# Performance work log

Hardware: AMD Instinct MI355X
Metric: run time of the kernel (lower is better)

The kernel has to match this reference:

```python
import jax, jax.numpy as jnp
import numpy as np

N_KERNELS = 21
N_LAYERS = 2
N_HEADS = 8
ATT_DIM = 32
FF_HID = 100
EMB = 300


def kernel_mus(n):
    mus = [1.0]
    bin_size = 2.0 / (n - 1)
    mus.append(1.0 - bin_size / 2.0)
    for _ in range(1, n - 1):
        mus.append(mus[-1] - bin_size)
    return np.array(mus, dtype=np.float32)


def kernel_sigmas(n):
    return np.array([0.001] + [0.1] * (n - 1), dtype=np.float32)


def setup_inputs() -> dict:
    key = jax.random.key(0)
    ks = jax.random.split(key, 12)
    B, LQ, LD = 32, 64, 512
    u = lambda k, s, a: jax.random.uniform(k, s, jnp.float32, -a, a)
    return dict(
        q_embed=jax.random.normal(ks[0], (B, LQ, EMB), jnp.float32),
        d_embed=jax.random.normal(ks[1], (B, LD, EMB), jnp.float32),
        mask_q=(jax.random.uniform(ks[2], (B, LQ)) > 0.1).astype(jnp.float32),
        mask_d=(jax.random.uniform(ks[3], (B, LD)) > 0.1).astype(jnp.float32),
        mixer=jnp.full((1, 1, 1), 0.5, jnp.float32),
        nn_scaler=jnp.full((1,), 0.01, jnp.float32),
        ff_w1=u(ks[4], (N_LAYERS, EMB, FF_HID), 0.05),
        ff_b1=jnp.zeros((N_LAYERS, FF_HID), jnp.float32),
        ff_w2=u(ks[5], (N_LAYERS, FF_HID, EMB), 0.05),
        ff_b2=jnp.zeros((N_LAYERS, EMB), jnp.float32),
        ln1_g=jnp.ones((N_LAYERS, EMB), jnp.float32),
        ln1_b=jnp.zeros((N_LAYERS, EMB), jnp.float32),
        att_w=u(ks[6], (N_LAYERS, EMB, 3 * ATT_DIM), 0.05),
        att_b=jnp.zeros((N_LAYERS, 3 * ATT_DIM), jnp.float32),
        out_w=u(ks[7], (N_LAYERS, ATT_DIM, EMB), 0.05),
        out_b=jnp.zeros((N_LAYERS, EMB), jnp.float32),
        ln2_g=jnp.ones((N_LAYERS, EMB), jnp.float32),
        ln2_b=jnp.zeros((N_LAYERS, EMB), jnp.float32),
        dense_w=u(ks[8], (1, N_KERNELS), 0.014),
    )


def _layer_norm(x, g, b, eps=1e-6):
    m = jnp.mean(x, -1, keepdims=True)
    s = jnp.std(x, -1, keepdims=True, ddof=1)  # torch std is unbiased
    return g * (x - m) / (s + eps) + b


def _encoder(x, mask, p):
    # AllenNLP StackedSelfAttentionEncoder: [FF -> res+LN -> MHSA -> res+LN] x2
    B, T, E = x.shape
    scale = jnp.sqrt(jnp.float32(E // N_HEADS))
    hd = ATT_DIM // N_HEADS
    for l in range(N_LAYERS):
        h = jax.nn.relu(x @ p['ff_w1'][l] + p['ff_b1'][l]) @ p['ff_w2'][l] + p['ff_b2'][l]
        h = _layer_norm(h + x, p['ln1_g'][l], p['ln1_b'][l])
        c = h @ p['att_w'][l] + p['att_b'][l]              # [B,T,3*ATT_DIM]
        q = c[..., :ATT_DIM].reshape(B, T, N_HEADS, hd)
        k = c[..., ATT_DIM:2 * ATT_DIM].reshape(B, T, N_HEADS, hd)
        v = c[..., 2 * ATT_DIM:].reshape(B, T, N_HEADS, hd)
        sims = jnp.einsum('bqhd,bkhd->bhqk', q / scale, k)
        m = mask[:, None, None, :]
        att = jax.nn.softmax(sims * m, axis=-1) * m         # AllenNLP masked_softmax
        att = att / (jnp.sum(att, -1, keepdims=True) + 1e-13)
        o = jnp.einsum('bhqk,bkhd->bqhd', att, v).reshape(B, T, ATT_DIM)
        o = o @ p['out_w'][l] + p['out_b'][l]
        x = _layer_norm(o + h, p['ln2_g'][l], p['ln2_b'][l])
    return x


def reference(q_embed, d_embed, mask_q, mask_d, mixer, nn_scaler,
              ff_w1, ff_b1, ff_w2, ff_b2, ln1_g, ln1_b,
              att_w, att_b, out_w, out_b, ln2_g, ln2_b, dense_w):
    p = dict(ff_w1=ff_w1, ff_b1=ff_b1, ff_w2=ff_w2, ff_b2=ff_b2,
             ln1_g=ln1_g, ln1_b=ln1_b, att_w=att_w, att_b=att_b,
             out_w=out_w, out_b=out_b, ln2_g=ln2_g, ln2_b=ln2_b)
    mu = jnp.asarray(kernel_mus(N_KERNELS))        # [K]
    sigma = jnp.asarray(kernel_sigmas(N_KERNELS))  # [K]
    mq = mask_q[..., None]
    md = mask_d[..., None]
    q = q_embed * mq
    d = d_embed * md
    qc = _encoder(q, mask_q, p)
    dc = _encoder(d, mask_d, p)
    q = (mixer * q + (1.0 - mixer) * qc) * mq
    d = (mixer * d + (1.0 - mixer) * dc) * md
    qd_mask = mask_q[:, :, None] * mask_d[:, None, :]  # [B,Q,D]
    qn = q / (jnp.linalg.norm(q, axis=-1, keepdims=True) + 1e-13)
    dn = d / (jnp.linalg.norm(d, axis=-1, keepdims=True) + 1e-13)
    cos = jnp.einsum('bqe,bde->bqd', qn, dn) * qd_mask
    # Gaussian RBF soft histogram: [B,Q,D,K]
    kr = jnp.exp(-(cos[..., None] - mu) ** 2 / (2.0 * sigma ** 2)) * qd_mask[..., None]
    pkq = jnp.sum(kr, axis=2)                                 # [B,Q,K]
    log_pkq = jnp.log2(jnp.clip(pkq, 1e-10)) * nn_scaler
    per_kernel = jnp.sum(log_pkq * mq, axis=1)                # [B,K]
    return jnp.squeeze(per_kernel @ dense_w.T, axis=1)        # [B]
```

## Files before the change

kernel.cpp:

```cpp
#include <hip/hip_runtime.h>
#include <hip/hip_bf16.h>

#define BATCH 32
#define LQ 64
#define LD 512
#define EMB 300
#define FFH 100
#define ATTD 32
#define NH 8
#define NK 21
#define MQ (BATCH * LQ)
#define MD (BATCH * LD)
#define MALL (MQ + MD)

typedef __attribute__((ext_vector_type(8))) short bf16x8;
typedef __attribute__((ext_vector_type(4))) float f32x4;

__device__ __forceinline__ float wave_sum(float v) {
    #pragma unroll
    for (int off = 32; off > 0; off >>= 1) v += __shfl_xor(v, off);
    return v;
}

__device__ __forceinline__ float bf2f(__hip_bfloat16 h) { return __bfloat162float(h); }

__device__ __forceinline__ float4 bf4_to_f4(const __hip_bfloat16* p) {
    uint2 u = *(const uint2*)p;
    float4 f;
    f.x = __uint_as_float((u.x & 0xffffu) << 16);
    f.y = __uint_as_float(u.x & 0xffff0000u);
    f.z = __uint_as_float((u.y & 0xffffu) << 16);
    f.w = __uint_as_float(u.y & 0xffff0000u);
    return f;
}

__device__ __forceinline__ unsigned short f2bfu(float x) {
    __hip_bfloat16 h = __float2bfloat16(x);
    return *(unsigned short*)&h;
}

__global__ void prep_all(const float* __restrict__ qe, const float* __restrict__ de,
                         const float* __restrict__ mq, const float* __restrict__ md,
                         const float* __restrict__ w1, const float* __restrict__ w2,
                         const float* __restrict__ aw, const float* __restrict__ ow,
                         __hip_bfloat16* __restrict__ xbf, float* __restrict__ mall,
                         __hip_bfloat16* __restrict__ w1t, __hip_bfloat16* __restrict__ w2t,
                         __hip_bfloat16* __restrict__ awt, __hip_bfloat16* __restrict__ owt) {
    int i = blockIdx.x * blockDim.x + threadIdx.x;
    const int NQ4 = MALL * (EMB / 4);
    if (i < NQ4) {
        int tok = i / (EMB / 4), c4 = (i % (EMB / 4)) * 4;
        float m;
        float4 v;
        if (tok < MQ) {
            m = mq[tok];
            v = *(const float4*)(qe + (size_t)tok * EMB + c4);
        } else {
            m = md[tok - MQ];
            v = *(const float4*)(de + (size_t)(tok - MQ) * EMB + c4);
        }
        uint2 u;
        u.x = (unsigned)f2bfu(v.x * m) | ((unsigned)f2bfu(v.y * m) << 16);
        u.y = (unsigned)f2bfu(v.z * m) | ((unsigned)f2bfu(v.w * m) << 16);
        *(uint2*)(xbf + (size_t)tok * EMB + c4) = u;
        if (c4 == 0) mall[tok] = m;
        return;
    }
    int j = i - NQ4;
    if (j < 2 * EMB * FFH) {
        int l = j / (EMB * FFH), r = j % (EMB * FFH);
        int k = r / FFH, n = r % FFH;
        w1t[(size_t)l * FFH * EMB + (size_t)n * EMB + k] = __float2bfloat16(w1[j]);
        return;
    }
    j -= 2 * EMB * FFH;
    if (j < 2 * 320 * 128) {
        int l = j / (320 * 128), r = j % (320 * 128);
        int n = r / 128, k = r % 128;
        float v = (n < EMB && k < FFH) ? w2[(size_t)l * FFH * EMB + (size_t)k * EMB + n] : 0.f;
        w2t[j] = __float2bfloat16(v);
        return;
    }
    j -= 2 * 320 * 128;
    if (j < 2 * EMB * 96) {
        int l = j / (EMB * 96), r = j % (EMB * 96);
        int k = r / 96, n = r % 96;
        awt[(size_t)l * 96 * EMB + (size_t)n * EMB + k] = __float2bfloat16(aw[j]);
        return;
    }
    j -= 2 * EMB * 96;
    if (j < 2 * 320 * 32) {
        int l = j / (320 * 32), r = j % (320 * 32);
        int n = r / 32, k = r % 32;
        float v = (n < EMB) ? ow[(size_t)l * ATTD * EMB + (size_t)k * EMB + n] : 0.f;
        owt[j] = __float2bfloat16(v);
    }
}

__device__ __forceinline__ void stage_row8(const __hip_bfloat16* __restrict__ src, bool rowvalid,
                                           int K, int gk, __hip_bfloat16* dst) {
    if (rowvalid && gk + 8 <= K) {
        const uint2* p = (const uint2*)(src + gk);
        uint2 a = p[0], b = p[1];
        *(uint2*)dst = a;
        *(uint2*)(dst + 4) = b;
    } else {
        #pragma unroll
        for (int j = 0; j < 8; j++)
            dst[j] = (rowvalid && gk + j < K) ? src[gk + j] : __float2bfloat16(0.f);
    }
}

template <bool RELU>
__global__ __launch_bounds__(256) void gemm_mfma(const __hip_bfloat16* __restrict__ A,
                                                 const __hip_bfloat16* __restrict__ Bt,
                                                 const float* __restrict__ bias,
                                                 __hip_bfloat16* __restrict__ Cb,
                                                 int M, int Nr, int Ns, int K) {
    __shared__ __align__(16) __hip_bfloat16 As[64][40];
    __shared__ __align__(16) __hip_bfloat16 Bs[64][40];
    const int tid = threadIdx.x;
    const int m0 = blockIdx.y * 64, n0 = blockIdx.x * 64;
    const int lane = tid & 63;
    const int wv = tid >> 6;
    const int wm = wv >> 1, wn = wv & 1;
    const int l15 = lane & 15, lg = lane >> 4;
    const int srow = tid >> 2, sk8 = (tid & 3) * 8;
    f32x4 acc[2][2] = {};
    const int NS = (K + 31) >> 5;
    const __hip_bfloat16* arow = A + (size_t)(m0 + srow) * K;
    const bool bvalid = (n0 + srow) < Nr;
    const __hip_bfloat16* brow = Bt + (size_t)(n0 + srow) * K;

    for (int s = 0; s < NS; s++) {
        const int gk = (s << 5) + sk8;
        if (s) __syncthreads();
        stage_row8(arow, true, K, gk, &As[srow][sk8]);
        stage_row8(brow, bvalid, K, gk, &Bs[srow][sk8]);
        __syncthreads();
        bf16x8 af0 = *(const bf16x8*)&As[wm * 32 + l15][lg * 8];
        bf16x8 af1 = *(const bf16x8*)&As[wm * 32 + 16 + l15][lg * 8];
        bf16x8 bf0 = *(const bf16x8*)&Bs[wn * 32 + l15][lg * 8];
        bf16x8 bf1 = *(const bf16x8*)&Bs[wn * 32 + 16 + l15][lg * 8];
        acc[0][0] = __builtin_amdgcn_mfma_f32_16x16x32_bf16(af0, bf0, acc[0][0], 0, 0, 0);
        acc[0][1] = __builtin_amdgcn_mfma_f32_16x16x32_bf16(af0, bf1, acc[0][1], 0, 0, 0);
        acc[1][0] = __builtin_amdgcn_mfma_f32_16x16x32_bf16(af1, bf0, acc[1][0], 0, 0, 0);
        acc[1][1] = __builtin_amdgcn_mfma_f32_16x16x32_bf16(af1, bf1, acc[1][1], 0, 0, 0);
    }

    #pragma unroll
    for (int fc = 0; fc < 2; fc++) {
        int col = n0 + wn * 32 + fc * 16 + l15;
        if (col >= Ns) continue;
        float bs = (col < Nr) ? bias[col] : 0.f;
        #pragma unroll
        for (int fr = 0; fr < 2; fr++) {
            int rbase = m0 + wm * 32 + fr * 16 + lg * 4;
            #pragma unroll
            for (int r = 0; r < 4; r++) {
                float v = acc[fr][fc][r] + bs;
                if (RELU) v = fmaxf(v, 0.f);
                Cb[(size_t)(rbase + r) * Ns + col] = __float2bfloat16(v);
            }
        }
    }
}

template <int NSTEP, int KSTR, int ASTR, bool MIX>
__global__ __launch_bounds__(256) void gemm_ln_direct(const __hip_bfloat16* __restrict__ A,
                                                      const __hip_bfloat16* __restrict__ Bt,
                                                      const float* __restrict__ bias,
                                                      const __hip_bfloat16* __restrict__ Res,
                                                      const float* __restrict__ g,
                                                      const float* __restrict__ beta,
                                                      __hip_bfloat16* __restrict__ Y,
                                                      const __hip_bfloat16* __restrict__ Xorig,
                                                      const float* __restrict__ mall,
                                                      const float* __restrict__ mixer) {
    const int tid = threadIdx.x;
    const int wv = tid >> 6;
    const int lane = tid & 63;
    const int l15 = lane & 15, lg = lane >> 4;
    const int m0 = blockIdx.x * 64 + wv * 16;

    f32x4 acc[19];
    #pragma unroll
    for (int fc = 0; fc < 19; fc++) acc[fc] = (f32x4){0.f, 0.f, 0.f, 0.f};

    #pragma unroll
    for (int ks = 0; ks < NSTEP; ks++) {
        const int kb = ks * 32 + lg * 8;
        bf16x8 af = *(const bf16x8*)(A + (size_t)(m0 + l15) * ASTR + kb);
        #pragma unroll
        for (int fc = 0; fc < 19; fc++) {
            bf16x8 bf = *(const bf16x8*)(Bt + (size_t)(fc * 16 + l15) * KSTR + kb);
            acc[fc] = __builtin_amdgcn_mfma_f32_16x16x32_bf16(af, bf, acc[fc], 0, 0, 0);
        }
    }

    float rs[4] = {0.f, 0.f, 0.f, 0.f};
    #pragma unroll
    for (int fc = 0; fc < 19; fc++) {
        int col = fc * 16 + l15;
        bool valid = col < EMB;
        float bs = valid ? bias[col] : 0.f;
        #pragma unroll
        for (int r = 0; r < 4; r++) {
            float v = 0.f;
            if (valid) v = acc[fc][r] + bs + bf2f(Res[(size_t)(m0 + lg * 4 + r) * EMB + col]);
            acc[fc][r] = v;
            rs[r] += v;
        }
    }
    #pragma unroll
    for (int r = 0; r < 4; r++)
        #pragma unroll
        for (int off = 1; off < 16; off <<= 1)
            rs[r] += __shfl_xor(rs[r], off);
    float mean[4], invv[4];
    #pragma unroll
    for (int r = 0; r < 4; r++) mean[r] = rs[r] * (1.f / EMB);

    float rq[4] = {0.f, 0.f, 0.f, 0.f};
    #pragma unroll
    for (int fc = 0; fc < 19; fc++) {
        int col = fc * 16 + l15;
        if (col < EMB) {
            #pragma unroll
            for (int r = 0; r < 4; r++) {
                float d = acc[fc][r] - mean[r];
                rq[r] += d * d;
            }
        }
    }
    #pragma unroll
    for (int r = 0; r < 4; r++) {
        #pragma unroll
        for (int off = 1; off < 16; off <<= 1)
            rq[r] += __shfl_xor(rq[r], off);
        float stdv = sqrtf(rq[r] * (1.f / (EMB - 1)));
        invv[r] = 1.f / (stdv + 1e-6f);
    }

    if (!MIX) {
        #pragma unroll
        for (int fc = 0; fc < 19; fc++) {
            int col = fc * 16 + l15;
            if (col >= EMB) continue;
            float gv = g[col], bv = beta[col];
            #pragma unroll
            for (int r = 0; r < 4; r++) {
                float y = gv * (acc[fc][r] - mean[r]) * invv[r] + bv;
                Y[(size_t)(m0 + lg * 4 + r) * EMB + col] = __float2bfloat16(y);
            }
        }
    } else {
        float mx = mixer[0];
        float mval[4];
        #pragma unroll
        for (int r = 0; r < 4; r++) mval[r] = mall[m0 + lg * 4 + r];
        float sq[4] = {0.f, 0.f, 0.f, 0.f};
        #pragma unroll
        for (int fc = 0; fc < 19; fc++) {
            int col = fc * 16 + l15;
            bool valid = col < EMB;
            float gv = valid ? g[col] : 0.f;
            float bv = valid ? beta[col] : 0.f;
            #pragma unroll
            for (int r = 0; r < 4; r++) {
                float v = 0.f;
                if (valid) {
                    float ln = gv * (acc[fc][r] - mean[r]) * invv[r] + bv;
                    float xo = bf2f(Xorig[(size_t)(m0 + lg * 4 + r) * EMB + col]);
                    v = (mx * xo + (1.f - mx) * ln) * mval[r];
                }
                acc[fc][r] = v;
                sq[r] += v * v;
            }
        }
        #pragma unroll
        for (int r = 0; r < 4; r++) {
            #pragma unroll
            for (int off = 1; off < 16; off <<= 1)
                sq[r] += __shfl_xor(sq[r], off);
            sq[r] = 1.f / (sqrtf(sq[r]) + 1e-13f);
        }
        #pragma unroll
        for (int fc = 0; fc < 19; fc++) {
            int col = fc * 16 + l15;
            if (col >= EMB) continue;
            #pragma unroll
            for (int r = 0; r < 4; r++) {
                Y[(size_t)(m0 + lg * 4 + r) * EMB + col] = __float2bfloat16(acc[fc][r] * sq[r]);
            }
        }
    }
}

__global__ __launch_bounds__(256) void cos_mfma(const __hip_bfloat16* __restrict__ Qn,
                                                const __hip_bfloat16* __restrict__ Dn,
                                                float* __restrict__ Cos) {
    __shared__ __align__(16) __hip_bfloat16 As[64][40];
    __shared__ __align__(16) __hip_bfloat16 Bs[64][40];
    const int b = blockIdx.y;
    const int n0 = blockIdx.x * 64;
    const int tid = threadIdx.x;
    const int lane = tid & 63;
    const int wv = tid >> 6;
    const int wm = wv >> 1, wn = wv & 1;
    const int l15 = lane & 15, lg = lane >> 4;
    const int srow = tid >> 2, sk8 = (tid & 3) * 8;
    f32x4 acc[2][2] = {};
    const int NS = (EMB + 31) >> 5;
    const __hip_bfloat16* arow = Qn + ((size_t)b * LQ + srow) * EMB;
    const __hip_bfloat16* brow = Dn + ((size_t)b * LD + n0 + srow) * EMB;

    for (int s = 0; s < NS; s++) {
        const int gk = (s << 5) + sk8;
        if (s) __syncthreads();
        stage_row8(arow, true, EMB, gk, &As[srow][sk8]);
        stage_row8(brow, true, EMB, gk, &Bs[srow][sk8]);
        __syncthreads();
        bf16x8 af0 = *(const bf16x8*)&As[wm * 32 + l15][lg * 8];
        bf16x8 af1 = *(const bf16x8*)&As[wm * 32 + 16 + l15][lg * 8];
        bf16x8 bf0 = *(const bf16x8*)&Bs[wn * 32 + l15][lg * 8];
        bf16x8 bf1 = *(const bf16x8*)&Bs[wn * 32 + 16 + l15][lg * 8];
        acc[0][0] = __builtin_amdgcn_mfma_f32_16x16x32_bf16(af0, bf0, acc[0][0], 0, 0, 0);
        acc[0][1] = __builtin_amdgcn_mfma_f32_16x16x32_bf16(af0, bf1, acc[0][1], 0, 0, 0);
        acc[1][0] = __builtin_amdgcn_mfma_f32_16x16x32_bf16(af1, bf0, acc[1][0], 0, 0, 0);
        acc[1][1] = __builtin_amdgcn_mfma_f32_16x16x32_bf16(af1, bf1, acc[1][1], 0, 0, 0);
    }

    float* cb = Cos + (size_t)b * LQ * LD;
    #pragma unroll
    for (int fc = 0; fc < 2; fc++) {
        int col = n0 + wn * 32 + fc * 16 + l15;
        #pragma unroll
        for (int fr = 0; fr < 2; fr++) {
            int rbase = wm * 32 + fr * 16 + lg * 4;
            #pragma unroll
            for (int r = 0; r < 4; r++) {
                cb[(size_t)(rbase + r) * LD + col] = acc[fr][fc][r];
            }
        }
    }
}

template <int T, int RPB, int KS>
__device__ __forceinline__ void attn_body(const __hip_bfloat16* __restrict__ cseg,
                                          const float* __restrict__ mask,
                                          __hip_bfloat16* __restrict__ oseg,
                                          int bh, int rb, char* smem) {
    constexpr int BLK = 512;
    float4* Ks = (float4*)smem;
    float4* Vs = Ks + T;
    float* part = (float*)(Vs + T);
    float* nmask_s = part + RPB * 5 * (KS - 1);
    const int b = bh / NH, h = bh % NH;
    const int tid = threadIdx.x;
    const __hip_bfloat16* base = cseg + (size_t)b * T * 96;

    if (tid == 0) *nmask_s = 0.f;
    __syncthreads();
    float lnm = 0.f;
    for (int j = tid; j < T; j += BLK) {
        float m = mask[b * T + j];
        float4 kv = bf4_to_f4(base + (size_t)j * 96 + ATTD + h * 4);
        float4 vv = bf4_to_f4(base + (size_t)j * 96 + 2 * ATTD + h * 4);
        kv.x *= m; kv.y *= m; kv.z *= m; kv.w *= m;
        vv.x *= m; vv.y *= m; vv.z *= m; vv.w *= m;
        Ks[j] = kv;
        Vs[j] = vv;
        lnm += 1.f - m;
    }
    lnm = wave_sum(lnm);
    if ((tid & 63) == 0 && lnm != 0.f) atomicAdd(nmask_s, lnm);
    __syncthreads();

    const int r = rb * RPB + (tid % RPB);
    const int ks = tid / RPB;
    const float inv_scale = 0.16439898730535729f;
    float4 qv = bf4_to_f4(base + (size_t)r * 96 + h * 4);
    qv.x *= inv_scale; qv.y *= inv_scale; qv.z *= inv_scale; qv.w *= inv_scale;

    float Sall = 0.f, ox = 0.f, oy = 0.f, oz = 0.f, ow = 0.f;
    constexpr int KC = T / KS;
    const int k0 = ks * KC;
    #pragma unroll 4
    for (int k = k0; k < k0 + KC; k++) {
        float4 kv = Ks[k];
        float4 vv = Vs[k];
        float s = fmaf(qv.x, kv.x, fmaf(qv.y, kv.y, fmaf(qv.z, kv.z, qv.w * kv.w)));
        float e = __expf(s);
        Sall += e;
        ox = fmaf(e, vv.x, ox);
        oy = fmaf(e, vv.y, oy);
        oz = fmaf(e, vv.z, oz);
        ow = fmaf(e, vv.w, ow);
    }
    if (ks > 0) {
        float* p = &part[((ks - 1) * RPB + (tid % RPB)) * 5];
        p[0] = Sall; p[1] = ox; p[2] = oy; p[3] = oz; p[4] = ow;
    }
    __syncthreads();
    if (ks == 0) {
        #pragma unroll
        for (int s2 = 0; s2 < KS - 1; s2++) {
            const float* p = &part[(s2 * RPB + r - rb * RPB) * 5];
            Sall += p[0]; ox += p[1]; oy += p[2]; oz += p[3]; ow += p[4];
        }
        float Sm = Sall - *nmask_s;
        float inv = 1.f / (Sm + 1e-13f * Sall);
        __hip_bfloat16* op = oseg + (size_t)(b * T + r) * ATTD + h * 4;
        op[0] = __float2bfloat16(ox * inv);
        op[1] = __float2bfloat16(oy * inv);
        op[2] = __float2bfloat16(oz * inv);
        op[3] = __float2bfloat16(ow * inv);
    }
}

__global__ __launch_bounds__(512) void attn_both(const __hip_bfloat16* __restrict__ cbf,
                                                 const float* __restrict__ mask_q,
                                                 const float* __restrict__ mask_d,
                                                 __hip_bfloat16* __restrict__ o32) {
    __shared__ __align__(16) char smem[24576];
    int blk = blockIdx.x;
    if (blk < BATCH * NH) {
        attn_body<LQ, 64, 8>(cbf, mask_q, o32, blk, 0, smem);
    } else {
        int bid = blk - BATCH * NH;
        attn_body<LD, 128, 4>(cbf + (size_t)MQ * 96, mask_d, o32 + (size_t)MQ * ATTD,
                              bid >> 2, bid & 3, smem);
    }
}

__global__ __launch_bounds__(256) void pool_kernel(const float* __restrict__ Cos,
                                                   const float* __restrict__ mask_q,
                                                   const float* __restrict__ mask_d,
                                                   const float* __restrict__ nn_scaler,
                                                   float* __restrict__ lp) {
    int wid = (blockIdx.x * 256 + threadIdx.x) >> 6;
    int lane = threadIdx.x & 63;
    int b = wid >> 6, qi = wid & 63;
    const float* crow = Cos + ((size_t)b * LQ + qi) * LD;
    const float* md = mask_d + b * LD;
    float acc[NK];
    #pragma unroll
    for (int k = 0; k < NK; k++) acc[k] = 0.f;
    #pragma unroll
    for (int rr = 0; rr < LD / 64; rr++) {
        int dj = rr * 64 + lane;
        float m = md[dj];
        if (m != 0.f) {
            float cv = crow[dj];
            float d0 = cv - 1.0f;
            acc[0] += __expf(d0 * d0 * -500000.0f);
            #pragma unroll
            for (int g = 0; g < 4; g++) {
                float mu_a = 0.95f - 0.5f * g;
                float dc = cv - mu_a;
                float t = __expf(dc * dc * -50.0f);
                float r = __expf(fmaf(-10.0f, dc, -0.5f));
                #pragma unroll
                for (int j = 0; j < 5; j++) {
                    acc[1 + 5 * g + j] += t;
                    t *= r;
                    r *= 0.36787944117144233f;
                }
            }
        }
    }
    float mq = mask_q[b * LQ + qi];
    float ns = nn_scaler[0];
    #pragma unroll
    for (int k = 0; k < NK; k++) {
        float s = wave_sum(acc[k]);
        if (lane == 0) lp[((size_t)b * LQ + qi) * NK + k] = log2f(fmaxf(s, 1e-10f)) * ns * mq;
    }
}

__global__ void final_kernel(const float* __restrict__ lp, const float* __restrict__ dense_w,
                             float* __restrict__ out) {
    int b = blockIdx.x;
    int t = threadIdx.x;
    float s = 0.f;
    if (t < NK) {
        for (int qi = 0; qi < LQ; qi++) s += lp[((size_t)b * LQ + qi) * NK + t];
        s *= dense_w[t];
    }
    s = wave_sum(s);
    if (t == 0) out[b] = s;
}

extern "C" void kernel_launch(void* const* d_in, const int* in_sizes, int n_in,
                              void* d_out, int out_size, void* d_ws, size_t ws_size,
                              hipStream_t stream) {
    (void)in_sizes; (void)n_in; (void)out_size; (void)ws_size;
    const float* q_embed  = (const float*)d_in[0];
    const float* d_embed  = (const float*)d_in[1];
    const float* mask_q   = (const float*)d_in[2];
    const float* mask_d   = (const float*)d_in[3];
    const float* mixer    = (const float*)d_in[4];
    const float* nn_scaler= (const float*)d_in[5];
    const float* ff_w1    = (const float*)d_in[6];
    const float* ff_b1    = (const float*)d_in[7];
    const float* ff_w2    = (const float*)d_in[8];
    const float* ff_b2    = (const float*)d_in[9];
    const float* ln1_g    = (const float*)d_in[10];
    const float* ln1_b    = (const float*)d_in[11];
    const float* att_w    = (const float*)d_in[12];
    const float* att_b    = (const float*)d_in[13];
    const float* out_w    = (const float*)d_in[14];
    const float* out_b    = (const float*)d_in[15];
    const float* ln2_g    = (const float*)d_in[16];
    const float* ln2_b    = (const float*)d_in[17];
    const float* dense_w  = (const float*)d_in[18];
    float* out = (float*)d_out;

    float* ws   = (float*)d_ws;
    float* cosb = ws;
    float* lp   = cosb + 1048576;
    float* mall = lp + 43008;
    __hip_bfloat16* xbf   = (__hip_bfloat16*)(mall + MALL);
    __hip_bfloat16* xcbf  = xbf  + (size_t)MALL * EMB;
    __hip_bfloat16* qdn   = xcbf + (size_t)MALL * EMB;
    __hip_bfloat16* hbf   = qdn  + (size_t)MALL * EMB;
    __hip_bfloat16* t1bf  = hbf  + (size_t)MALL * EMB;
    __hip_bfloat16* cbf   = t1bf + (size_t)MALL * 128;
    __hip_bfloat16* o32bf = cbf  + (size_t)MALL * 96;
    __hip_bfloat16* w1t   = o32bf + (size_t)MALL * ATTD;
    __hip_bfloat16* w2t   = w1t + 2 * FFH * EMB;
    __hip_bfloat16* awt   = w2t + 2 * 320 * 128;
    __hip_bfloat16* owt   = awt + 2 * 96 * EMB;

    const int PREP_N = MALL * (EMB / 4) + 2 * EMB * FFH + 2 * 320 * 128 + 2 * EMB * 96 + 2 * 320 * 32;
    prep_all<<<(PREP_N + 255) / 256, 256, 0, stream>>>(
        q_embed, d_embed, mask_q, mask_d, ff_w1, ff_w2, att_w, out_w,
        xbf, mall, w1t, w2t, awt, owt);

    const __hip_bfloat16* xcur = xbf;
    for (int l = 0; l < 2; l++) {
        gemm_mfma<true><<<dim3(2, MALL / 64), 256, 0, stream>>>(
            xcur, w1t + (size_t)l * FFH * EMB, ff_b1 + l * FFH, t1bf, MALL, FFH, 128, EMB);
        gemm_ln_direct<4, 128, 128, false><<<MALL / 64, 256, 0, stream>>>(
            t1bf, w2t + (size_t)l * 320 * 128, ff_b2 + l * EMB, xcur,
            ln1_g + l * EMB, ln1_b + l * EMB, hbf, nullptr, nullptr, nullptr);
        gemm_mfma<false><<<dim3(2, MALL / 64), 256, 0, stream>>>(
            hbf, awt + (size_t)l * 96 * EMB, att_b + l * 96, cbf, MALL, 96, 96, EMB);
        attn_both<<<BATCH * NH + BATCH * NH * (LD / 128), 512, 0, stream>>>(
            cbf, mask_q, mask_d, o32bf);
        if (l == 0) {
            gemm_ln_direct<1, 32, 32, false><<<MALL / 64, 256, 0, stream>>>(
                o32bf, owt, out_b, hbf, ln2_g, ln2_b, xcbf, nullptr, nullptr, nullptr);
            xcur = xcbf;
        } else {
            gemm_ln_direct<1, 32, 32, true><<<MALL / 64, 256, 0, stream>>>(
                o32bf, owt + (size_t)320 * 32, out_b + EMB, hbf,
                ln2_g + EMB, ln2_b + EMB, qdn, xbf, mall, mixer);
        }
    }

    cos_mfma<<<dim3(LD / 64, BATCH), 256, 0, stream>>>(qdn, qdn + (size_t)MQ * EMB, cosb);

    pool_kernel<<<(BATCH * LQ) / 4, 256, 0, stream>>>(cosb, mask_q, mask_d, nn_scaler, lp);

    final_kernel<<<BATCH, 64, 0, stream>>>(lp, dense_w, out);
}
```

Measured before the change: 233.3 us.

## Store cosine matrix in bf16 and fuse final reduction into pool via atomic counter

The cosine similarity matrix is now written and read as bf16 instead of fp32, halving that intermediate's memory traffic. The final dense reduction kernel is removed. The last wave per batch, found with an atomic counter that prep_all resets, does the dense dot product inside the pool kernel, saving one launch. This risks precision loss in the RBF histogram, where sigma=0.001 for the exact-match kernel makes bf16 rounding of cos near 1 significant.

```diff
diff --git a/kernel.cpp b/kernel.cpp
--- a/kernel.cpp
+++ b/kernel.cpp
@@ -45,7 +45,8 @@
                          const float* __restrict__ aw, const float* __restrict__ ow,
                          __hip_bfloat16* __restrict__ xbf, float* __restrict__ mall,
                          __hip_bfloat16* __restrict__ w1t, __hip_bfloat16* __restrict__ w2t,
-                         __hip_bfloat16* __restrict__ awt, __hip_bfloat16* __restrict__ owt) {
+                         __hip_bfloat16* __restrict__ awt, __hip_bfloat16* __restrict__ owt,
+                         int* __restrict__ cnt) {
     int i = blockIdx.x * blockDim.x + threadIdx.x;
     const int NQ4 = MALL * (EMB / 4);
     if (i < NQ4) {
@@ -94,7 +95,10 @@
         int n = r / 32, k = r % 32;
         float v = (n < EMB) ? ow[(size_t)l * ATTD * EMB + (size_t)k * EMB + n] : 0.f;
         owt[j] = __float2bfloat16(v);
-    }
+        return;
+    }
+    j -= 2 * 320 * 32;
+    if (j < BATCH) cnt[j] = 0;
 }
 
 __device__ __forceinline__ void stage_row8(const __hip_bfloat16* __restrict__ src, bool rowvalid,
@@ -299,7 +303,7 @@
 
 __global__ __launch_bounds__(256) void cos_mfma(const __hip_bfloat16* __restrict__ Qn,
                                                 const __hip_bfloat16* __restrict__ Dn,
-                                                float* __restrict__ Cos) {
+                                                __hip_bfloat16* __restrict__ Cos) {
     __shared__ __align__(16) __hip_bfloat16 As[64][40];
     __shared__ __align__(16) __hip_bfloat16 Bs[64][40];
     const int b = blockIdx.y;
@@ -331,7 +335,7 @@
         acc[1][1] = __builtin_amdgcn_mfma_f32_16x16x32_bf16(af1, bf1, acc[1][1], 0, 0, 0);
     }
 
-    float* cb = Cos + (size_t)b * LQ * LD;
+    __hip_bfloat16* cb = Cos + (size_t)b * LQ * LD;
     #pragma unroll
     for (int fc = 0; fc < 2; fc++) {
         int col = n0 + wn * 32 + fc * 16 + l15;
@@ -340,7 +344,7 @@
             int rbase = wm * 32 + fr * 16 + lg * 4;
             #pragma unroll
             for (int r = 0; r < 4; r++) {
-                cb[(size_t)(rbase + r) * LD + col] = acc[fr][fc][r];
+                cb[(size_t)(rbase + r) * LD + col] = __float2bfloat16(acc[fr][fc][r]);
             }
         }
     }
@@ -434,15 +438,18 @@
     }
 }
 
-__global__ __launch_bounds__(256) void pool_kernel(const float* __restrict__ Cos,
-                                                   const float* __restrict__ mask_q,
-                                                   const float* __restrict__ mask_d,
-                                                   const float* __restrict__ nn_scaler,
-                                                   float* __restrict__ lp) {
+__global__ __launch_bounds__(256) void pool_final(const __hip_bfloat16* __restrict__ Cos,
+                                                  const float* __restrict__ mask_q,
+                                                  const float* __restrict__ mask_d,
+                                                  const float* __restrict__ nn_scaler,
+                                                  const float* __restrict__ dense_w,
+                                                  float* __restrict__ lp,
+                                                  int* __restrict__ cnt,
+                                                  float* __restrict__ out) {
     int wid = (blockIdx.x * 256 + threadIdx.x) >> 6;
     int lane = threadIdx.x & 63;
     int b = wid >> 6, qi = wid & 63;
-    const float* crow = Cos + ((size_t)b * LQ + qi) * LD;
+    const __hip_bfloat16* crow = Cos + ((size_t)b * LQ + qi) * LD;
     const float* md = mask_d + b * LD;
     float acc[NK];
     #pragma unroll
@@ -452,7 +459,7 @@
         int dj = rr * 64 + lane;
         float m = md[dj];
         if (m != 0.f) {
-            float cv = crow[dj];
+            float cv = bf2f(crow[dj]);
             float d0 = cv - 1.0f;
             acc[0] += __expf(d0 * d0 * -500000.0f);
             #pragma unroll
@@ -477,19 +484,20 @@
         float s = wave_sum(acc[k]);
         if (lane == 0) lp[((size_t)b * LQ + qi) * NK + k] = log2f(fmaxf(s, 1e-10f)) * ns * mq;
     }
-}
-
-__global__ void final_kernel(const float* __restrict__ lp, const float* __restrict__ dense_w,
-                             float* __restrict__ out) {
-    int b = blockIdx.x;
-    int t = threadIdx.x;
-    float s = 0.f;
-    if (t < NK) {
-        for (int qi = 0; qi < LQ; qi++) s += lp[((size_t)b * LQ + qi) * NK + t];
-        s *= dense_w[t];
-    }
-    s = wave_sum(s);
-    if (t == 0) out[b] = s;
+
+    __threadfence();
+    int old = 0;
+    if (lane == 0) old = atomicAdd(&cnt[b], 1);
+    old = __shfl(old, 0);
+    if (old == LQ - 1) {
+        __threadfence();
+        const float* lpb = lp + (size_t)b * LQ * NK;
+        float t = 0.f;
+        #pragma unroll
+        for (int k = 0; k < NK; k++) t += lpb[(size_t)lane * NK + k] * dense_w[k];
+        t = wave_sum(t);
+        if (lane == 0) out[b] = t;
+    }
 }
 
 extern "C" void kernel_launch(void* const* d_in, const int* in_sizes, int n_in,
@@ -518,10 +526,11 @@
     float* out = (float*)d_out;
 
     float* ws   = (float*)d_ws;
-    float* cosb = ws;
-    float* lp   = cosb + 1048576;
+    float* lp   = ws;
     float* mall = lp + 43008;
-    __hip_bfloat16* xbf   = (__hip_bfloat16*)(mall + MALL);
+    int*   cnt  = (int*)(mall + MALL);
+    __hip_bfloat16* cosbf = (__hip_bfloat16*)(cnt + BATCH);
+    __hip_bfloat16* xbf   = cosbf + (size_t)BATCH * LQ * LD;
     __hip_bfloat16* xcbf  = xbf  + (size_t)MALL * EMB;
     __hip_bfloat16* qdn   = xcbf + (size_t)MALL * EMB;
     __hip_bfloat16* hbf   = qdn  + (size_t)MALL * EMB;
@@ -533,10 +542,11 @@
     __hip_bfloat16* awt   = w2t + 2 * 320 * 128;
     __hip_bfloat16* owt   = awt + 2 * 96 * EMB;
 
-    const int PREP_N = MALL * (EMB / 4) + 2 * EMB * FFH + 2 * 320 * 128 + 2 * EMB * 96 + 2 * 320 * 32;
+    const int PREP_N = MALL * (EMB / 4) + 2 * EMB * FFH + 2 * 320 * 128 + 2 * EMB * 96
+                     + 2 * 320 * 32 + BATCH;
     prep_all<<<(PREP_N + 255) / 256, 256, 0, stream>>>(
         q_embed, d_embed, mask_q, mask_d, ff_w1, ff_w2, att_w, out_w,
-        xbf, mall, w1t, w2t, awt, owt);
+        xbf, mall, w1t, w2t, awt, owt, cnt);
 
     const __hip_bfloat16* xcur = xbf;
     for (int l = 0; l < 2; l++) {
@@ -560,9 +570,8 @@
         }
     }
 
-    cos_mfma<<<dim3(LD / 64, BATCH), 256, 0, stream>>>(qdn, qdn + (size_t)MQ * EMB, cosb);
-
-    pool_kernel<<<(BATCH * LQ) / 4, 256, 0, stream>>>(cosb, mask_q, mask_d, nn_scaler, lp);
-
-    final_kernel<<<BATCH, 64, 0, stream>>>(lp, dense_w, out);
-}
+    cos_mfma<<<dim3(LD / 64, BATCH), 256, 0, stream>>>(qdn, qdn + (size_t)MQ * EMB, cosbf);
+
+    pool_final<<<(BATCH * LQ) / 4, 256, 0, stream>>>(cosbf, mask_q, mask_d, nn_scaler,
+                                                     dense_w, lp, cnt, out);
+}
```

New measurement: 294.6 us. 26.3% more time.
